# Performance work log

Hardware: AMD Instinct MI355X
Metric: run time of the kernel (lower is better)

The kernel has to match this reference:

```python
import jax, jax.numpy as jnp
import numpy as np

H = 128      # hidden_dim
N = 200000   # number of available (job, machine) ops
M = 1000     # machine nodes
J = 5000     # job nodes


def setup_inputs() -> dict:
    key = jax.random.key(0)
    ks = jax.random.split(key, 8)
    s = 0.05  # weight scale
    return {
        "x_graph": jax.random.normal(ks[0], (1, 2 * H), jnp.float32),
        "x_m": jax.random.normal(ks[1], (M, H), jnp.float32),
        "x_job": jax.random.normal(ks[2], (J, H), jnp.float32),
        "m_ids": jax.random.randint(ks[3], (N,), 0, M),
        "job_idx": jax.random.randint(ks[4], (N,), 0, J),
        "W0": jax.random.normal(ks[5], (4 * H, H), jnp.float32) * s,
        "b0": jnp.zeros((H,), jnp.float32),
        "W1": jax.random.normal(ks[6], (H, H), jnp.float32) * s,
        "b1": jnp.zeros((H,), jnp.float32),
        "W2": jax.random.normal(ks[7], (H, 1), jnp.float32) * s,
        "b2": jnp.zeros((1,), jnp.float32),
    }


def reference(x_graph, x_m, x_job, m_ids, job_idx, W0, b0, W1, b1, W2, b2):
    n = m_ids.shape[0]
    # vectorized form of the python loop: [x_graph | x_m[m_id] | x_job[job_pos]] -> [N, 4H]
    feats = jnp.concatenate(
        [
            jnp.broadcast_to(x_graph, (n, x_graph.shape[1])),
            x_m[m_ids],
            x_job[job_idx],
        ],
        axis=1,
    )
    h = jax.nn.relu(feats @ W0 + b0)   # Linear(4H -> H) + ReLU
    h = jax.nn.relu(h @ W1 + b1)       # Linear(H -> H) + ReLU
    scores = (h @ W2 + b2)[:, 0]       # Linear(H -> 1), squeeze -> [N]
    logp = jax.nn.log_softmax(scores, axis=0)
    probs = jnp.exp(logp)
    idx = jnp.argmax(scores)           # greedy selection (deterministic baseline)
    entropy = -jnp.sum(probs * logp)   # Categorical entropy
    return idx, probs[idx], logp[idx], entropy
```

## Files before the change

kernel.cpp:

```cpp
#include <hip/hip_runtime.h>
#include <math.h>

#define HID 128
#define TILE_R 64
#define XS_STRIDE 132
#define H0S_STRIDE 136
#define DELTA 0.05f

typedef short bf16x8 __attribute__((ext_vector_type(8)));
typedef float f32x4 __attribute__((ext_vector_type(4)));

static __device__ __forceinline__ unsigned short f2bf(float f) {
    union { float f; unsigned u; } v; v.f = f;
    unsigned r = v.u + 0x7FFFu + ((v.u >> 16) & 1u);
    return (unsigned short)(r >> 16);
}
static __device__ __forceinline__ float bflo(unsigned u) {
    union { unsigned u; float f; } v; v.u = u << 16; return v.f;
}
static __device__ __forceinline__ float bfhi(unsigned u) {
    union { unsigned u; float f; } v; v.u = u & 0xFFFF0000u; return v.f;
}

#define FMA4(avc, wv)                         \
    acc[r][0] = fmaf(avc, wv.x, acc[r][0]);   \
    acc[r][1] = fmaf(avc, wv.y, acc[r][1]);   \
    acc[r][2] = fmaf(avc, wv.z, acc[r][2]);   \
    acc[r][3] = fmaf(avc, wv.w, acc[r][3]);

__global__ __launch_bounds__(256, 4) void precompute_kernel(
    const float* __restrict__ x_graph,
    const float* __restrict__ x_m,
    const float* __restrict__ x_job,
    const float* __restrict__ W0,
    const float* __restrict__ b0,
    const float* __restrict__ W1,
    float* __restrict__ g,
    unsigned short* __restrict__ Pbf,
    unsigned short* __restrict__ W1T,
    int M, int J, int aTiles, int bTiles)
{
    const int t = threadIdx.x;
    const int bid = blockIdx.x;

    if (bid == 0) {
        __shared__ float xg[2 * HID];
        if (t < HID) { xg[t] = x_graph[t]; xg[t + HID] = x_graph[t + HID]; }
        __syncthreads();
        if (t < HID) {
            float acc = b0[t];
            #pragma unroll 8
            for (int k = 0; k < 2 * HID; ++k)
                acc = fmaf(xg[k], W0[k * HID + t], acc);
            g[t] = acc;
        }
        return;
    }
    if (bid == 1 + aTiles + bTiles) {
        for (int e = t; e < HID * HID; e += 256) {
            int n = e >> 7, k = e & 127;
            W1T[e] = f2bf(W1[k * HID + n]);
        }
        return;
    }

    const int tb = bid - 1;
    const float* X;
    const float* W;
    int r0, nr, dstBase;
    if (tb < aTiles) {
        r0 = tb * TILE_R;
        nr = min(TILE_R, M - r0);
        X = x_m + (size_t)r0 * HID;
        W = W0 + 2 * HID * HID;
        dstBase = r0;
    } else {
        int jb = tb - aTiles;
        r0 = jb * TILE_R;
        nr = min(TILE_R, J - r0);
        X = x_job + (size_t)r0 * HID;
        W = W0 + 3 * HID * HID;
        dstBase = M + r0;
    }

    __shared__ float xs[TILE_R * XS_STRIDE];
    {
        int row = t >> 2;
        int q = t & 3;
        #pragma unroll
        for (int u = 0; u < 8; ++u) {
            int c = q * 32 + u * 4;
            float4 v = (row < nr) ? *(const float4*)(X + row * HID + c)
                                  : make_float4(0.f, 0.f, 0.f, 0.f);
            *(float4*)&xs[row * XS_STRIDE + c] = v;
        }
    }
    __syncthreads();

    const int w = t >> 6;
    const int l = t & 63;
    const int tc = l & 7;
    const int tr = l >> 3;
    const int c0 = w * 32 + tc * 4;

    float acc[8][4];
    #pragma unroll
    for (int r = 0; r < 8; ++r)
        #pragma unroll
        for (int c = 0; c < 4; ++c) acc[r][c] = 0.0f;

    #pragma unroll 2
    for (int k0 = 0; k0 < HID; k0 += 4) {
        float4 w0v = *(const float4*)(W + (k0 + 0) * HID + c0);
        float4 w1v = *(const float4*)(W + (k0 + 1) * HID + c0);
        float4 w2m = *(const float4*)(W + (k0 + 2) * HID + c0);
        float4 w3v = *(const float4*)(W + (k0 + 3) * HID + c0);
        #pragma unroll
        for (int r = 0; r < 8; ++r) {
            float4 a = *(const float4*)&xs[(r * 8 + tr) * XS_STRIDE + k0];
            FMA4(a.x, w0v)
            FMA4(a.y, w1v)
            FMA4(a.z, w2m)
            FMA4(a.w, w3v)
        }
    }

    #pragma unroll
    for (int r = 0; r < 8; ++r) {
        int row = r * 8 + tr;
        if (row < nr) {
            unsigned lo0 = (unsigned)f2bf(acc[r][0]) | ((unsigned)f2bf(acc[r][1]) << 16);
            unsigned lo1 = (unsigned)f2bf(acc[r][2]) | ((unsigned)f2bf(acc[r][3]) << 16);
            uint2 pk = make_uint2(lo0, lo1);
            *(uint2*)(Pbf + (size_t)(dstBase + row) * HID + c0) = pk;
        }
    }
}

__global__ __launch_bounds__(256, 3) void main_kernel(
    const int* __restrict__ m_ids,
    const int* __restrict__ job_idx,
    const float* __restrict__ b1,
    const float* __restrict__ W2,
    const float* __restrict__ b2,
    const float* __restrict__ g,
    const unsigned short* __restrict__ Pbf,
    const unsigned short* __restrict__ W1T,
    float* __restrict__ scores,
    float4* __restrict__ partials,
    int N, int M)
{
    __shared__ __align__(16) short h0s[TILE_R * H0S_STRIDE];
    __shared__ __align__(16) short w1s[HID * H0S_STRIDE];
    __shared__ float sred[TILE_R];

    const int t = threadIdx.x;
    const int row0 = blockIdx.x * TILE_R;

    {
        const uint4* src = (const uint4*)W1T;
        #pragma unroll
        for (int e = t; e < 2048; e += 256) {
            int n = e >> 4, pos = e & 15;
            *(uint4*)&w1s[n * H0S_STRIDE + pos * 8] = src[e];
        }
    }

    {
        int row = t >> 2;
        int q = t & 3;
        int grow = row0 + row;
        int gr = (grow < N) ? grow : (N - 1);
        int m = m_ids[gr];
        int j = job_idx[gr];
        const unsigned short* pm = Pbf + (size_t)m * HID + q * 32;
        const unsigned short* pj = Pbf + (size_t)(M + j) * HID + q * 32;
        const float* gp = g + q * 32;
        short* dst = &h0s[row * H0S_STRIDE + q * 32];
        #pragma unroll
        for (int u = 0; u < 4; ++u) {
            uint4 mv = *(const uint4*)(pm + u * 8);
            uint4 jv = *(const uint4*)(pj + u * 8);
            float4 g0 = *(const float4*)(gp + u * 8);
            float4 g1 = *(const float4*)(gp + u * 8 + 4);
            float h0v = fmaxf(bflo(mv.x) + bflo(jv.x) + g0.x, 0.f);
            float h1v = fmaxf(bfhi(mv.x) + bfhi(jv.x) + g0.y, 0.f);
            float h2v = fmaxf(bflo(mv.y) + bflo(jv.y) + g0.z, 0.f);
            float h3v = fmaxf(bfhi(mv.y) + bfhi(jv.y) + g0.w, 0.f);
            float h4v = fmaxf(bflo(mv.z) + bflo(jv.z) + g1.x, 0.f);
            float h5v = fmaxf(bfhi(mv.z) + bfhi(jv.z) + g1.y, 0.f);
            float h6v = fmaxf(bflo(mv.w) + bflo(jv.w) + g1.z, 0.f);
            float h7v = fmaxf(bfhi(mv.w) + bfhi(jv.w) + g1.w, 0.f);
            uint4 pk;
            pk.x = (unsigned)f2bf(h0v) | ((unsigned)f2bf(h1v) << 16);
            pk.y = (unsigned)f2bf(h2v) | ((unsigned)f2bf(h3v) << 16);
            pk.z = (unsigned)f2bf(h4v) | ((unsigned)f2bf(h5v) << 16);
            pk.w = (unsigned)f2bf(h6v) | ((unsigned)f2bf(h7v) << 16);
            *(uint4*)(dst + u * 8) = pk;
        }
    }
    __syncthreads();

    const int l = t & 63;
    const int w = t >> 6;
    const int quad = l >> 4;
    const int mrow = l & 15;

    bf16x8 af[4];
    const short* ab = &h0s[(w * 16 + mrow) * H0S_STRIDE + quad * 8];
    #pragma unroll
    for (int kc = 0; kc < 4; ++kc)
        af[kc] = *(const bf16x8*)(ab + kc * 32);

    f32x4 acc[8];
    #pragma unroll
    for (int nt = 0; nt < 8; ++nt) {
        f32x4 z = {0.f, 0.f, 0.f, 0.f};
        acc[nt] = z;
    }

    const short* bb = &w1s[mrow * H0S_STRIDE + quad * 8];
    #pragma unroll
    for (int nt = 0; nt < 8; ++nt) {
        #pragma unroll
        for (int kc = 0; kc < 4; ++kc) {
            bf16x8 bfr = *(const bf16x8*)(bb + nt * 16 * H0S_STRIDE + kc * 32);
            acc[nt] = __builtin_amdgcn_mfma_f32_16x16x32_bf16(af[kc], bfr, acc[nt], 0, 0, 0);
        }
    }

    float p0 = 0.f, p1 = 0.f, p2 = 0.f, p3 = 0.f;
    #pragma unroll
    for (int nt = 0; nt < 8; ++nt) {
        int c = nt * 16 + mrow;
        float b1v = b1[c], w2v = W2[c];
        p0 += fmaxf(acc[nt][0] + b1v, 0.f) * w2v;
        p1 += fmaxf(acc[nt][1] + b1v, 0.f) * w2v;
        p2 += fmaxf(acc[nt][2] + b1v, 0.f) * w2v;
        p3 += fmaxf(acc[nt][3] + b1v, 0.f) * w2v;
    }
    #pragma unroll
    for (int off = 1; off < 16; off <<= 1) {
        p0 += __shfl_xor(p0, off);
        p1 += __shfl_xor(p1, off);
        p2 += __shfl_xor(p2, off);
        p3 += __shfl_xor(p3, off);
    }
    if (mrow == 0) {
        int rb = w * 16 + quad * 4;
        sred[rb + 0] = p0;
        sred[rb + 1] = p1;
        sred[rb + 2] = p2;
        sred[rb + 3] = p3;
    }
    __syncthreads();

    if (t < 64) {
        int grow = row0 + t;
        float s = sred[t] + b2[0];
        if (grow < N) scores[grow] = s;
        else s = -1e30f;

        float mmax = s;
        int midx = grow;
        #pragma unroll
        for (int off = 1; off < 64; off <<= 1) {
            float om = __shfl_xor(mmax, off);
            int oi = __shfl_xor(midx, off);
            if (om > mmax || (om == mmax && oi < midx)) { mmax = om; midx = oi; }
        }
        float d = s - mmax;
        float e = expf(d);
        float z = e;
        float ss = d * e;
        #pragma unroll
        for (int off = 1; off < 64; off <<= 1) {
            z += __shfl_xor(z, off);
            ss += __shfl_xor(ss, off);
        }
        if (t == 0)
            partials[blockIdx.x] = make_float4(mmax, z, ss, (float)midx);
    }
}

__device__ inline void sm_merge(float& am, float& az, float& ass, int& ai,
                                float bm, float bz, float bss, int bi)
{
    if (bm > am || (bm == am && bi < ai)) {
        float tm = am, tz = az, ts = ass; int ti = ai;
        am = bm; az = bz; ass = bss; ai = bi;
        bm = tm; bz = tz; bss = ts; bi = ti;
    }
    float f = expf(bm - am);
    az += bz * f;
    ass += (bss + (bm - am) * bz) * f;
}

__global__ __launch_bounds__(1024) void merge_kernel(
    const float4* __restrict__ partials, int nparts,
    float* __restrict__ statsf, float* __restrict__ out)
{
    __shared__ float4 wred[16];
    __shared__ int widx[16];
    const int t = threadIdx.x;
    const int w = t >> 6;
    const int l = t & 63;

    float m = -1e30f, z = 0.f, ss = 0.f;
    int idx = 0x7fffffff;
    for (int i = t; i < nparts; i += 1024) {
        float4 p = partials[i];
        sm_merge(m, z, ss, idx, p.x, p.y, p.z, (int)p.w);
    }
    #pragma unroll
    for (int off = 1; off < 64; off <<= 1) {
        float om = __shfl_xor(m, off);
        float oz = __shfl_xor(z, off);
        float os = __shfl_xor(ss, off);
        int oi = __shfl_xor(idx, off);
        sm_merge(m, z, ss, idx, om, oz, os, oi);
    }
    if (l == 0) { wred[w] = make_float4(m, z, ss, 0.f); widx[w] = idx; }
    __syncthreads();
    if (t == 0) {
        for (int i = 1; i < 16; ++i)
            sm_merge(m, z, ss, idx, wred[i].x, wred[i].y, wred[i].z, widx[i]);
        out[3] = logf(z) - ss / z;
        statsf[0] = m;
        statsf[1] = z;
    }
}

__global__ __launch_bounds__(256) void scan_kernel(
    const float* __restrict__ scores,
    const float* __restrict__ statsf,
    const int* __restrict__ m_ids,
    const int* __restrict__ job_idx,
    const float* __restrict__ x_m,
    const float* __restrict__ x_job,
    const float* __restrict__ W0,
    const float* __restrict__ W1,
    const float* __restrict__ b1,
    const float* __restrict__ W2,
    const float* __restrict__ b2,
    const float* __restrict__ g,
    float2* __restrict__ bests,
    int N)
{
    __shared__ int cand[256];
    __shared__ int ccount;
    __shared__ float rs[4];
    __shared__ int ri[4];

    const int t = threadIdx.x;
    const int w = t >> 6;
    const int l = t & 63;
    const int base = blockIdx.x * 256;

    if (t == 0) ccount = 0;
    __syncthreads();

    const float cut = statsf[0] - DELTA;
    int i = base + t;
    if (i < N && scores[i] >= cut) {
        int p = atomicAdd(&ccount, 1);
        cand[p] = i;
    }
    __syncthreads();
    const int nc = ccount;
    if (nc == 0) {
        if (t == 0) bests[blockIdx.x] = make_float2(-1e30f, __int_as_float(0x7fffffff));
        return;
    }

    float bs = -1e30f;
    int bi = 0x7fffffff;
    for (int c = w; c < nc; c += 4) {
        int gr = cand[c];
        int mm = m_ids[gr];
        int jj = job_idx[gr];
        const float* xm = x_m + (size_t)mm * HID;
        const float* xj = x_job + (size_t)jj * HID;
        const float* wm = W0 + 2 * HID * HID;
        const float* wj = W0 + 3 * HID * HID;
        float a0 = g[l], a1 = g[l + 64];
        for (int k = 0; k < HID; ++k) {
            float xmk = xm[k];
            float xjk = xj[k];
            a0 = fmaf(xmk, wm[k * HID + l], a0);
            a1 = fmaf(xmk, wm[k * HID + l + 64], a1);
            a0 = fmaf(xjk, wj[k * HID + l], a0);
            a1 = fmaf(xjk, wj[k * HID + l + 64], a1);
        }
        a0 = fmaxf(a0, 0.f);
        a1 = fmaxf(a1, 0.f);
        float acc0 = 0.f, acc1 = 0.f;
        for (int k = 0; k < 64; ++k) {
            float h = __shfl(a0, k);
            acc0 = fmaf(h, W1[k * HID + l], acc0);
            acc1 = fmaf(h, W1[k * HID + l + 64], acc1);
        }
        for (int k = 0; k < 64; ++k) {
            float h = __shfl(a1, k);
            acc0 = fmaf(h, W1[(k + 64) * HID + l], acc0);
            acc1 = fmaf(h, W1[(k + 64) * HID + l + 64], acc1);
        }
        float p = fmaxf(acc0 + b1[l], 0.f) * W2[l]
                + fmaxf(acc1 + b1[l + 64], 0.f) * W2[l + 64];
        #pragma unroll
        for (int off = 1; off < 64; off <<= 1)
            p += __shfl_xor(p, off);
        float s = p + b2[0];
        if (s > bs || (s == bs && gr < bi)) { bs = s; bi = gr; }
    }
    if (l == 0) { rs[w] = bs; ri[w] = bi; }
    __syncthreads();
    if (t == 0) {
        float best = rs[0];
        int bwin = ri[0];
        for (int i2 = 1; i2 < 4; ++i2)
            if (rs[i2] > best || (rs[i2] == best && ri[i2] < bwin)) {
                best = rs[i2]; bwin = ri[i2];
            }
        bests[blockIdx.x] = make_float2(best, __int_as_float(bwin));
    }
}

__global__ __launch_bounds__(256) void finalize_kernel(
    const float2* __restrict__ bests, int nblocks,
    const float* __restrict__ statsf,
    float* __restrict__ out)
{
    __shared__ float rs[4];
    __shared__ int ri[4];
    const int t = threadIdx.x;
    const int w = t >> 6;
    const int l = t & 63;

    float bs = -1e30f;
    int bi = 0x7fffffff;
    for (int i = t; i < nblocks; i += 256) {
        float2 b = bests[i];
        int gi = __float_as_int(b.y);
        if (b.x > bs || (b.x == bs && gi < bi)) { bs = b.x; bi = gi; }
    }
    #pragma unroll
    for (int off = 1; off < 64; off <<= 1) {
        float os = __shfl_xor(bs, off);
        int oi = __shfl_xor(bi, off);
        if (os > bs || (os == bs && oi < bi)) { bs = os; bi = oi; }
    }
    if (l == 0) { rs[w] = bs; ri[w] = bi; }
    __syncthreads();
    if (t == 0) {
        for (int i = 1; i < 4; ++i)
            if (rs[i] > bs || (rs[i] == bs && ri[i] < bi)) { bs = rs[i]; bi = ri[i]; }
        float mhat = statsf[0], Z = statsf[1];
        out[0] = (float)bi;
        out[1] = expf(bs - mhat) / Z;
        out[2] = (bs - mhat) - logf(Z);
    }
}

extern "C" void kernel_launch(void* const* d_in, const int* in_sizes, int n_in,
                              void* d_out, int out_size, void* d_ws, size_t ws_size,
                              hipStream_t stream)
{
    const float* x_graph = (const float*)d_in[0];
    const float* x_m     = (const float*)d_in[1];
    const float* x_job   = (const float*)d_in[2];
    const int*   m_ids   = (const int*)d_in[3];
    const int*   job_idx = (const int*)d_in[4];
    const float* W0      = (const float*)d_in[5];
    const float* b0      = (const float*)d_in[6];
    const float* W1      = (const float*)d_in[7];
    const float* b1      = (const float*)d_in[8];
    const float* W2      = (const float*)d_in[9];
    const float* b2      = (const float*)d_in[10];
    float* out = (float*)d_out;

    const int N = in_sizes[3];
    const int M = in_sizes[1] / HID;
    const int J = in_sizes[2] / HID;

    const int tiles = (N + TILE_R - 1) / TILE_R;
    const int aTiles = (M + TILE_R - 1) / TILE_R;
    const int bTiles = (J + TILE_R - 1) / TILE_R;
    const int sblocks = (N + 255) / 256;

    float* ws = (float*)d_ws;
    float* g = ws;
    float* scores = ws + HID;
    float4* partials = (float4*)(scores + N);
    float* statsf = (float*)(partials + tiles);
    float2* bests = (float2*)(statsf + 4);
    unsigned short* W1T = (unsigned short*)(bests + sblocks + (sblocks & 1));
    unsigned short* Pbf = W1T + HID * HID;

    precompute_kernel<<<1 + aTiles + bTiles + 1, 256, 0, stream>>>(
        x_graph, x_m, x_job, W0, b0, W1, g, Pbf, W1T, M, J, aTiles, bTiles);
    main_kernel<<<tiles, 256, 0, stream>>>(
        m_ids, job_idx, b1, W2, b2, g, Pbf, W1T, scores, partials, N, M);
    merge_kernel<<<1, 1024, 0, stream>>>(partials, tiles, statsf, out);
    scan_kernel<<<sblocks, 256, 0, stream>>>(
        scores, statsf, m_ids, job_idx, x_m, x_job, W0, W1, b1, W2, b2, g,
        bests, N);
    finalize_kernel<<<1, 256, 0, stream>>>(bests, sblocks, statsf, out);
}
```

Measured before the change: 155.1 us.

## Drop merge kernel by folding max into scan blocks and softmax merge into finalize

Removes the single-block merge_kernel launch. Each scan block now reduces the max over all per-tile partials itself to get its candidate cutoff, and finalize_kernel does the full online-softmax merge (Z, entropy) alongside the argmax reduction. Separately, the precompute projection tile shrinks from 64 to 32 rows so more blocks cover the x_m and x_job projections. The trade-off is that each of the ~780 scan blocks redundantly reads all ~3125 partials, in exchange for one fewer serialized launch.

```diff
diff --git a/kernel.cpp b/kernel.cpp
--- a/kernel.cpp
+++ b/kernel.cpp
@@ -3,6 +3,7 @@
 
 #define HID 128
 #define TILE_R 64
+#define TILE_P 32
 #define XS_STRIDE 132
 #define H0S_STRIDE 136
 #define DELTA 0.05f
@@ -69,27 +70,27 @@
     const float* W;
     int r0, nr, dstBase;
     if (tb < aTiles) {
-        r0 = tb * TILE_R;
-        nr = min(TILE_R, M - r0);
+        r0 = tb * TILE_P;
+        nr = min(TILE_P, M - r0);
         X = x_m + (size_t)r0 * HID;
         W = W0 + 2 * HID * HID;
         dstBase = r0;
     } else {
         int jb = tb - aTiles;
-        r0 = jb * TILE_R;
-        nr = min(TILE_R, J - r0);
+        r0 = jb * TILE_P;
+        nr = min(TILE_P, J - r0);
         X = x_job + (size_t)r0 * HID;
         W = W0 + 3 * HID * HID;
         dstBase = M + r0;
     }
 
-    __shared__ float xs[TILE_R * XS_STRIDE];
+    __shared__ float xs[TILE_P * XS_STRIDE];
     {
-        int row = t >> 2;
-        int q = t & 3;
-        #pragma unroll
-        for (int u = 0; u < 8; ++u) {
-            int c = q * 32 + u * 4;
+        int row = t >> 3;
+        int e = t & 7;
+        #pragma unroll
+        for (int u = 0; u < 4; ++u) {
+            int c = e * 16 + u * 4;
             float4 v = (row < nr) ? *(const float4*)(X + row * HID + c)
                                   : make_float4(0.f, 0.f, 0.f, 0.f);
             *(float4*)&xs[row * XS_STRIDE + c] = v;
@@ -103,9 +104,9 @@
     const int tr = l >> 3;
     const int c0 = w * 32 + tc * 4;
 
-    float acc[8][4];
-    #pragma unroll
-    for (int r = 0; r < 8; ++r)
+    float acc[4][4];
+    #pragma unroll
+    for (int r = 0; r < 4; ++r)
         #pragma unroll
         for (int c = 0; c < 4; ++c) acc[r][c] = 0.0f;
 
@@ -116,7 +117,7 @@
         float4 w2m = *(const float4*)(W + (k0 + 2) * HID + c0);
         float4 w3v = *(const float4*)(W + (k0 + 3) * HID + c0);
         #pragma unroll
-        for (int r = 0; r < 8; ++r) {
+        for (int r = 0; r < 4; ++r) {
             float4 a = *(const float4*)&xs[(r * 8 + tr) * XS_STRIDE + k0];
             FMA4(a.x, w0v)
             FMA4(a.y, w1v)
@@ -126,7 +127,7 @@
     }
 
     #pragma unroll
-    for (int r = 0; r < 8; ++r) {
+    for (int r = 0; r < 4; ++r) {
         int row = r * 8 + tr;
         if (row < nr) {
             unsigned lo0 = (unsigned)f2bf(acc[r][0]) | ((unsigned)f2bf(acc[r][1]) << 16);
@@ -296,44 +297,9 @@
     ass += (bss + (bm - am) * bz) * f;
 }
 
-__global__ __launch_bounds__(1024) void merge_kernel(
+__global__ __launch_bounds__(256) void scan_kernel(
     const float4* __restrict__ partials, int nparts,
-    float* __restrict__ statsf, float* __restrict__ out)
-{
-    __shared__ float4 wred[16];
-    __shared__ int widx[16];
-    const int t = threadIdx.x;
-    const int w = t >> 6;
-    const int l = t & 63;
-
-    float m = -1e30f, z = 0.f, ss = 0.f;
-    int idx = 0x7fffffff;
-    for (int i = t; i < nparts; i += 1024) {
-        float4 p = partials[i];
-        sm_merge(m, z, ss, idx, p.x, p.y, p.z, (int)p.w);
-    }
-    #pragma unroll
-    for (int off = 1; off < 64; off <<= 1) {
-        float om = __shfl_xor(m, off);
-        float oz = __shfl_xor(z, off);
-        float os = __shfl_xor(ss, off);
-        int oi = __shfl_xor(idx, off);
-        sm_merge(m, z, ss, idx, om, oz, os, oi);
-    }
-    if (l == 0) { wred[w] = make_float4(m, z, ss, 0.f); widx[w] = idx; }
-    __syncthreads();
-    if (t == 0) {
-        for (int i = 1; i < 16; ++i)
-            sm_merge(m, z, ss, idx, wred[i].x, wred[i].y, wred[i].z, widx[i]);
-        out[3] = logf(z) - ss / z;
-        statsf[0] = m;
-        statsf[1] = z;
-    }
-}
-
-__global__ __launch_bounds__(256) void scan_kernel(
     const float* __restrict__ scores,
-    const float* __restrict__ statsf,
     const int* __restrict__ m_ids,
     const int* __restrict__ job_idx,
     const float* __restrict__ x_m,
@@ -351,16 +317,25 @@
     __shared__ int ccount;
     __shared__ float rs[4];
     __shared__ int ri[4];
+    __shared__ float mmx[4];
 
     const int t = threadIdx.x;
     const int w = t >> 6;
     const int l = t & 63;
     const int base = blockIdx.x * 256;
 
+    float mhat = -1e30f;
+    for (int i = t; i < nparts; i += 256)
+        mhat = fmaxf(mhat, partials[i].x);
+    #pragma unroll
+    for (int off = 1; off < 64; off <<= 1)
+        mhat = fmaxf(mhat, __shfl_xor(mhat, off));
+    if (l == 0) mmx[w] = mhat;
     if (t == 0) ccount = 0;
     __syncthreads();
-
-    const float cut = statsf[0] - DELTA;
+    mhat = fmaxf(fmaxf(mmx[0], mmx[1]), fmaxf(mmx[2], mmx[3]));
+    const float cut = mhat - DELTA;
+
     int i = base + t;
     if (i < N && scores[i] >= cut) {
         int p = atomicAdd(&ccount, 1);
@@ -427,15 +402,33 @@
 }
 
 __global__ __launch_bounds__(256) void finalize_kernel(
+    const float4* __restrict__ partials, int nparts,
     const float2* __restrict__ bests, int nblocks,
-    const float* __restrict__ statsf,
     float* __restrict__ out)
 {
+    __shared__ float4 wred[4];
+    __shared__ int widx[4];
     __shared__ float rs[4];
     __shared__ int ri[4];
     const int t = threadIdx.x;
     const int w = t >> 6;
     const int l = t & 63;
+
+    float m = -1e30f, z = 0.f, ss = 0.f;
+    int idx = 0x7fffffff;
+    for (int i = t; i < nparts; i += 256) {
+        float4 p = partials[i];
+        sm_merge(m, z, ss, idx, p.x, p.y, p.z, (int)p.w);
+    }
+    #pragma unroll
+    for (int off = 1; off < 64; off <<= 1) {
+        float om = __shfl_xor(m, off);
+        float oz = __shfl_xor(z, off);
+        float os = __shfl_xor(ss, off);
+        int oi = __shfl_xor(idx, off);
+        sm_merge(m, z, ss, idx, om, oz, os, oi);
+    }
+    if (l == 0) { wred[w] = make_float4(m, z, ss, 0.f); widx[w] = idx; }
 
     float bs = -1e30f;
     int bi = 0x7fffffff;
@@ -452,13 +445,17 @@
     }
     if (l == 0) { rs[w] = bs; ri[w] = bi; }
     __syncthreads();
+
     if (t == 0) {
-        for (int i = 1; i < 4; ++i)
+        for (int i = 1; i < 4; ++i) {
+            sm_merge(m, z, ss, idx, wred[i].x, wred[i].y, wred[i].z, widx[i]);
             if (rs[i] > bs || (rs[i] == bs && ri[i] < bi)) { bs = rs[i]; bi = ri[i]; }
-        float mhat = statsf[0], Z = statsf[1];
+        }
+        float logZ = logf(z);
         out[0] = (float)bi;
-        out[1] = expf(bs - mhat) / Z;
-        out[2] = (bs - mhat) - logf(Z);
+        out[1] = expf(bs - m) / z;
+        out[2] = (bs - m) - logZ;
+        out[3] = logZ - ss / z;
     }
 }
 
@@ -484,16 +481,15 @@
     const int J = in_sizes[2] / HID;
 
     const int tiles = (N + TILE_R - 1) / TILE_R;
-    const int aTiles = (M + TILE_R - 1) / TILE_R;
-    const int bTiles = (J + TILE_R - 1) / TILE_R;
+    const int aTiles = (M + TILE_P - 1) / TILE_P;
+    const int bTiles = (J + TILE_P - 1) / TILE_P;
     const int sblocks = (N + 255) / 256;
 
     float* ws = (float*)d_ws;
     float* g = ws;
     float* scores = ws + HID;
     float4* partials = (float4*)(scores + N);
-    float* statsf = (float*)(partials + tiles);
-    float2* bests = (float2*)(statsf + 4);
+    float2* bests = (float2*)(partials + tiles);
     unsigned short* W1T = (unsigned short*)(bests + sblocks + (sblocks & 1));
     unsigned short* Pbf = W1T + HID * HID;
 
@@ -501,9 +497,8 @@
         x_graph, x_m, x_job, W0, b0, W1, g, Pbf, W1T, M, J, aTiles, bTiles);
     main_kernel<<<tiles, 256, 0, stream>>>(
         m_ids, job_idx, b1, W2, b2, g, Pbf, W1T, scores, partials, N, M);
-    merge_kernel<<<1, 1024, 0, stream>>>(partials, tiles, statsf, out);
     scan_kernel<<<sblocks, 256, 0, stream>>>(
-        scores, statsf, m_ids, job_idx, x_m, x_job, W0, W1, b1, W2, b2, g,
-        bests, N);
-    finalize_kernel<<<1, 256, 0, stream>>>(bests, sblocks, statsf, out);
-}
+        partials, tiles, scores, m_ids, job_idx, x_m, x_job, W0, W1, b1, W2, b2,
+        g, bests, N);
+    finalize_kernel<<<1, 256, 0, stream>>>(partials, tiles, bests, sblocks, out);
+}
```

Result: faster. 145.0 us (-6.5%).
